# Performance work log

Hardware: AMD Instinct MI355X
Metric: run time of the kernel (lower is better)

## Reference

```python
import jax, jax.numpy as jnp
import numpy as np

D_MODEL = 2048
NUM_HEADS = 16
HEAD_DIM = D_MODEL // NUM_HEADS  # 128; scale uses head_dim even though attention is over full d_model
B, S = 2, 2048


def setup_inputs() -> dict:
    key = jax.random.key(0)
    ks = jax.random.split(key, 5)
    x = jax.random.normal(ks[0], (B, S, D_MODEL), dtype=jnp.float32)
    # causal additive mask, as typically passed to this module (2D, sliced mask[-s:, :kv])
    neg = jnp.float32(-1e9)
    mask = jnp.where(jnp.triu(jnp.ones((S, S), dtype=bool), k=1), neg, jnp.float32(0.0))
    std = 1.0 / np.sqrt(D_MODEL)
    Wq = jax.random.normal(ks[1], (D_MODEL, D_MODEL), dtype=jnp.float32) * std
    Wk = jax.random.normal(ks[2], (D_MODEL, D_MODEL), dtype=jnp.float32) * std
    Wv = jax.random.normal(ks[3], (D_MODEL, D_MODEL), dtype=jnp.float32) * std
    Wo = jax.random.normal(ks[4], (D_MODEL, D_MODEL), dtype=jnp.float32) * std
    return {"x": x, "mask": mask, "Wq": Wq, "Wk": Wk, "Wv": Wv, "Wo": Wo}


def reference(x, mask, Wq, Wk, Wv, Wo):
    # nn.Linear(bias=False): y = x @ W^T
    q = jnp.einsum('bsd,ed->bse', x, Wq)  # [B,S,D]
    k = jnp.einsum('bsd,ed->bse', x, Wk)
    v = jnp.einsum('bsd,ed->bse', x, Wv)
    scale = jnp.float32(HEAD_DIM ** -0.5)
    # NOTE: faithful to source — contraction over full d_model, no head split
    scores = jnp.einsum('bsd,btd->bst', q, k) * scale  # [B,S,S]
    scores = scores + mask  # mask[-s:, :kv] == mask here (s == kv)
    weights = jax.nn.softmax(scores, axis=-1)
    out = jnp.einsum('bst,btd->bsd', weights, v)
    return jnp.einsum('bsd,ed->bse', out, Wo)
```

## Files before the change

kernel.cpp:

```cpp
#include <hip/hip_runtime.h>

#define DM  2048
#define SQ  2048
#define NB  2
#define BSZ (NB * SQ)

typedef _Float16 f16x8 __attribute__((ext_vector_type(8)));
typedef __attribute__((ext_vector_type(4))) float f32x4;

#define ASG(p) (const __attribute__((address_space(1))) void*)(p)
#define ASL(p) (__attribute__((address_space(3))) void*)(p)

__device__ __forceinline__ unsigned short f2h(float f) {
  union { _Float16 h; unsigned short u; } x;
  x.h = (_Float16)f;
  return x.u;
}
__device__ __forceinline__ float h2f(unsigned short u) {
  union { unsigned short u; _Float16 h; } x;
  x.u = u;
  return (float)x.h;
}

__global__ __launch_bounds__(256) void cast_x_wo(const float4* __restrict__ x,
                                                 const float4* __restrict__ wo,
                                                 ushort4* __restrict__ outx,
                                                 ushort4* __restrict__ outwo,
                                                 int n4x, int n4w) {
  int i = blockIdx.x * 256 + threadIdx.x;
  float4 v;
  ushort4* dst;
  int j;
  if (i < n4x) { v = x[i]; dst = outx; j = i; }
  else { j = i - n4x; if (j >= n4w) return; v = wo[j]; dst = outwo; }
  ushort4 h;
  h.x = f2h(v.x); h.y = f2h(v.y); h.z = f2h(v.z); h.w = f2h(v.w);
  dst[j] = h;
}

__global__ __launch_bounds__(256) void cast_t(const float* __restrict__ wq,
                                              const float* __restrict__ wk,
                                              const float* __restrict__ wv,
                                              unsigned short* __restrict__ wqT,
                                              unsigned short* __restrict__ wkT,
                                              unsigned short* __restrict__ wvT) {
  __shared__ unsigned short tile[64][66];
  const float* in = (blockIdx.z == 0) ? wq : (blockIdx.z == 1) ? wk : wv;
  unsigned short* outT = (blockIdx.z == 0) ? wqT : (blockIdx.z == 1) ? wkT : wvT;
  const int tid = threadIdx.x;
  const int d0 = blockIdx.x * 64, e0 = blockIdx.y * 64;
  const int r = tid >> 4;
  const int c = (tid & 15) * 4;
#pragma unroll
  for (int p = 0; p < 4; p++) {
    const int dl = r + p * 16;
    float4 v = *(const float4*)&in[(long)(d0 + dl) * DM + e0 + c];
    tile[c + 0][dl] = f2h(v.x);
    tile[c + 1][dl] = f2h(v.y);
    tile[c + 2][dl] = f2h(v.z);
    tile[c + 3][dl] = f2h(v.w);
  }
  __syncthreads();
  const int r2 = tid >> 3;
  const int c2 = (tid & 7) * 8;
#pragma unroll
  for (int p = 0; p < 2; p++) {
    const int el = r2 + p * 32;
    union { uint4 u4; unsigned short us[8]; } o;
#pragma unroll
    for (int k = 0; k < 8; k++) o.us[k] = tile[el][c2 + k];
    *(uint4*)&outT[(long)(e0 + el) * DM + d0 + c2] = o.u4;
  }
}

#define SB() __builtin_amdgcn_sched_barrier(0)
#define BARX() do { SB(); __builtin_amdgcn_s_barrier(); SB(); } while (0)

#define STAGEK(BUFL, REG, U, T) do { \
    const unsigned short* G_ = (REG) ? Bb : Ab; \
    const int ldG_ = (REG) ? ldB : ldA; \
    const int r0_ = ((REG) ? bn0 : bm0) + (U) * 32; \
    const long k0_ = (long)((T) << 6); \
    char* db_ = ldsb + (BUFL) * 32768 + (REG) * 16384 + (U) * 4096 + tid * 16; \
    const unsigned short* s_ = G_ + (long)(r0_ + srow) * ldG_ + k0_ + scsw; \
    __builtin_amdgcn_global_load_lds(ASG(s_), ASL(db_), 16, 0, 0); \
  } while (0)

#define LDAK(BUFL, MH, Af) do { \
    const char* ba_ = ldsb + (BUFL) * 32768 + (wm * 64 + (MH) * 32) * 128 + arow; \
    _Pragma("unroll") for (int mm_ = 0; mm_ < 2; mm_++) { \
      Af[mm_][0] = *(const f16x8*)(ba_ + mm_ * 2048 + sl0); \
      Af[mm_][1] = *(const f16x8*)(ba_ + mm_ * 2048 + sl1); } \
  } while (0)

#define LDBK(BUFL, NH, Bf) do { \
    const char* bb_ = ldsb + (BUFL) * 32768 + 16384 + (wn * 64 + (NH) * 32) * 128 + arow; \
    _Pragma("unroll") for (int nn_ = 0; nn_ < 2; nn_++) { \
      Bf[nn_][0] = *(const f16x8*)(bb_ + nn_ * 2048 + sl0); \
      Bf[nn_][1] = *(const f16x8*)(bb_ + nn_ * 2048 + sl1); } \
  } while (0)

#define PHK(Af, Bf, MH, NH) do { \
    __builtin_amdgcn_s_setprio(1); \
    _Pragma("unroll") for (int mm_ = 0; mm_ < 2; mm_++) \
    _Pragma("unroll") for (int nn_ = 0; nn_ < 2; nn_++) \
    _Pragma("unroll") for (int ks_ = 0; ks_ < 2; ks_++) \
      acc[(MH) * 2 + mm_][(NH) * 2 + nn_] = __builtin_amdgcn_mfma_f32_16x16x32_f16( \
          Af[mm_][ks_], Bf[nn_][ks_], acc[(MH) * 2 + mm_][(NH) * 2 + nn_], 0, 0, 0); \
    __builtin_amdgcn_s_setprio(0); \
  } while (0)

#define GROUPK(BUFL, T) do { \
    LDAK(BUFL, 0, a0); LDBK(BUFL, 0, b0); \
    LDAK(BUFL, 1, a1); \
    if ((T) + 1 < NT) { STAGEK((BUFL) ^ 1, 1, 2, (T) + 1); STAGEK((BUFL) ^ 1, 1, 3, (T) + 1); } \
    PHK(a0, b0, 0, 0); \
    BARX(); \
    LDBK(BUFL, 1, b1); \
    PHK(a1, b0, 1, 0); \
    BARX(); \
    if ((T) + 2 < NT) { STAGEK(BUFL, 0, 0, (T) + 2); STAGEK(BUFL, 0, 1, (T) + 2); \
                        STAGEK(BUFL, 0, 2, (T) + 2); STAGEK(BUFL, 0, 3, (T) + 2); } \
    PHK(a1, b1, 1, 1); \
    BARX(); \
    if ((T) + 2 < NT) { STAGEK(BUFL, 1, 0, (T) + 2); STAGEK(BUFL, 1, 1, (T) + 2); } \
    PHK(a0, b1, 0, 1); \
    SB(); \
    if ((T) + 1 < NT) { \
      if ((T) + 1 == NT - 1) { asm volatile("s_waitcnt vmcnt(0)" ::: "memory"); } \
      else                   { asm volatile("s_waitcnt vmcnt(6)" ::: "memory"); } \
    } \
    __builtin_amdgcn_s_barrier(); \
    SB(); \
  } while (0)

template <int OM>
__device__ __forceinline__ void gemm128_body(
    char* ldsb, const unsigned short* __restrict__ Ab,
    const unsigned short* __restrict__ Bb,
    float* __restrict__ Cf, unsigned short* __restrict__ Ch, long cb,
    int NT, int ldA, int ldB, int ldC, int bm0, int bn0, float alpha) {
  const int tid = threadIdx.x, lane = tid & 63, wid = tid >> 6;
  const int wm = wid >> 1, wn = wid & 1;
  const int fr = lane & 15, fq = lane >> 4;

  const int sl0 = ((fq ^ (fr & 7)) << 4);
  const int sl1 = (((4 + fq) ^ (fr & 7)) << 4);
  const int arow = fr << 7;

  const int srow = tid >> 3;
  const int scsw = ((tid & 7) ^ (srow & 7)) << 3;

  f32x4 acc[4][4];
#pragma unroll
  for (int m = 0; m < 4; m++)
#pragma unroll
    for (int n = 0; n < 4; n++)
#pragma unroll
      for (int r = 0; r < 4; r++) acc[m][n][r] = 0.f;

  f16x8 a0[2][2], a1[2][2], b0[2][2], b1[2][2];

  STAGEK(0, 0, 0, 0); STAGEK(0, 0, 1, 0); STAGEK(0, 0, 2, 0); STAGEK(0, 0, 3, 0);
  STAGEK(0, 1, 0, 0); STAGEK(0, 1, 1, 0); STAGEK(0, 1, 2, 0); STAGEK(0, 1, 3, 0);
  STAGEK(1, 0, 0, 1); STAGEK(1, 0, 1, 1); STAGEK(1, 0, 2, 1); STAGEK(1, 0, 3, 1);
  STAGEK(1, 1, 0, 1); STAGEK(1, 1, 1, 1);
  asm volatile("s_waitcnt vmcnt(6)" ::: "memory");
  __builtin_amdgcn_s_barrier();
  SB();

  for (int t = 0; t < NT; t += 2) {
    GROUPK(0, t);
    GROUPK(1, t + 1);
  }

#pragma unroll
  for (int mh = 0; mh < 2; mh++)
#pragma unroll
    for (int mm = 0; mm < 2; mm++)
#pragma unroll
      for (int nh = 0; nh < 2; nh++)
#pragma unroll
        for (int nn = 0; nn < 2; nn++) {
          const int col = bn0 + wn * 64 + nh * 32 + nn * 16 + fr;
#pragma unroll
          for (int r = 0; r < 4; r++) {
            const long row = (long)bm0 + wm * 64 + mh * 32 + mm * 16 + fq * 4 + r;
            const long ci = cb + row * ldC + col;
            const float vv = acc[mh * 2 + mm][nh * 2 + nn][r] * alpha;
            if constexpr (OM == 0) Cf[ci] = vv;
            else                   Ch[ci] = f2h(vv);
          }
        }
}

template <int OM, int CAUSAL>
__global__ __launch_bounds__(256, 2) void gemm128(
    const unsigned short* __restrict__ A, const unsigned short* __restrict__ B,
    float* __restrict__ Cf, unsigned short* __restrict__ Ch,
    int K, long sAb, long sBb, long sCb,
    int ldA, int ldB, int ldC, float alpha) {
  __shared__ __align__(16) char ldsarr[65536];
  const int bm0 = blockIdx.x * 128;
  const int bn0 = blockIdx.y * 128;
  if (CAUSAL == 1 && bn0 > bm0) return;
  const int z = blockIdx.z;
  int NT = K >> 6;
  if (CAUSAL == 2) NT = (bm0 + 128) >> 6;
  gemm128_body<OM>(ldsarr, A + (long)z * sAb, B + (long)z * sBb,
                   Cf, Ch, (long)z * sCb, NT, ldA, ldB, ldC, bm0, bn0, alpha);
}

__global__ __launch_bounds__(256, 2) void k_mt_g(
    const unsigned short* __restrict__ wkT, const unsigned short* __restrict__ wqT,
    const unsigned short* __restrict__ wo16, const unsigned short* __restrict__ wvT,
    unsigned short* __restrict__ MT, unsigned short* __restrict__ G) {
  __shared__ __align__(16) char ldsarr[65536];
  const int bm0 = blockIdx.x * 128;
  const int bn0 = blockIdx.y * 128;
  if (blockIdx.z == 0)
    gemm128_body<1>(ldsarr, wkT, wqT, nullptr, MT, 0L, DM >> 6, DM, DM, DM, bm0, bn0, 1.0f);
  else
    gemm128_body<1>(ldsarr, wo16, wvT, nullptr, G, 0L, DM >> 6, DM, DM, DM, bm0, bn0, 1.0f);
}

__global__ __launch_bounds__(256, 2) void k_y_ut(
    const unsigned short* __restrict__ x16, const unsigned short* __restrict__ MT,
    const unsigned short* __restrict__ G,
    unsigned short* __restrict__ y, unsigned short* __restrict__ uT) {
  __shared__ __align__(16) char ldsarr[65536];
  if (blockIdx.z == 0) {
    const int bm0 = blockIdx.x * 128;
    const int bn0 = blockIdx.y * 128;
    gemm128_body<1>(ldsarr, x16, MT, nullptr, y, 0L, DM >> 6, DM, DM, DM, bm0, bn0, 1.0f);
  } else {
    const int bm0 = blockIdx.y * 128;
    const int bn0 = blockIdx.x * 128;
    gemm128_body<1>(ldsarr, G, x16, nullptr, uT, 0L, DM >> 6, DM, DM, BSZ, bm0, bn0, 1.0f);
  }
}

__global__ __launch_bounds__(256) void softmax_causal(const unsigned short* __restrict__ sc,
                                                      unsigned short* __restrict__ pr) {
  const int row = blockIdx.x;
  const int s = row & (SQ - 1);
  const long base = (long)row * SQ;
  const int n = s + 1;
  const int tid = threadIdx.x;
  const int lane = tid & 63;
  const int wv = tid >> 6;
  const int e0 = tid * 8;
  __shared__ float red[4];

  union { uint4 u4; unsigned short us[8]; } in, ou;
  in.u4 = *(const uint4*)&sc[base + e0];

  float v[8];
  float mx = -3.0e38f;
#pragma unroll
  for (int j = 0; j < 8; j++) {
    v[j] = (e0 + j < n) ? h2f(in.us[j]) : -3.0e38f;
    mx = fmaxf(mx, v[j]);
  }
#pragma unroll
  for (int o = 32; o >= 1; o >>= 1) mx = fmaxf(mx, __shfl_xor(mx, o));
  if (lane == 0) red[wv] = mx;
  __syncthreads();
  mx = fmaxf(fmaxf(red[0], red[1]), fmaxf(red[2], red[3]));
  __syncthreads();

  float sum = 0.f;
#pragma unroll
  for (int j = 0; j < 8; j++) {
    v[j] = (e0 + j < n) ? __expf(v[j] - mx) : 0.f;
    sum += v[j];
  }
#pragma unroll
  for (int o = 32; o >= 1; o >>= 1) sum += __shfl_xor(sum, o);
  if (lane == 0) red[wv] = sum;
  __syncthreads();
  const float inv = 1.f / (red[0] + red[1] + red[2] + red[3]);
#pragma unroll
  for (int j = 0; j < 8; j++) ou.us[j] = (e0 + j < n) ? f2h(v[j] * inv) : (unsigned short)0;
  *(uint4*)&pr[base + e0] = ou.u4;
}

extern "C" void kernel_launch(void* const* d_in, const int* in_sizes, int n_in,
                              void* d_out, int out_size, void* d_ws, size_t ws_size,
                              hipStream_t stream) {
  (void)in_sizes; (void)n_in; (void)out_size; (void)ws_size;
  const float* x  = (const float*)d_in[0];
  const float* Wq = (const float*)d_in[2];
  const float* Wk = (const float*)d_in[3];
  const float* Wv = (const float*)d_in[4];
  const float* Wo = (const float*)d_in[5];
  float* out = (float*)d_out;

  const long ELx = (long)BSZ * DM;
  const long ELw = (long)DM * DM;

  char* ws = (char*)d_ws;
  size_t off = 0;
  auto take = [&](size_t bytes) { void* p = ws + off; off += bytes; return p; };

  unsigned short* x16  = (unsigned short*)take(ELx * 2);
  unsigned short* wqT  = (unsigned short*)take(ELw * 2);
  unsigned short* wkT  = (unsigned short*)take(ELw * 2);
  unsigned short* wvT  = (unsigned short*)take(ELw * 2);
  unsigned short* wo16 = (unsigned short*)take(ELw * 2);
  unsigned short* MT   = (unsigned short*)take(ELw * 2);
  unsigned short* G    = (unsigned short*)take(ELw * 2);
  unsigned short* y    = (unsigned short*)take(ELx * 2);
  unsigned short* uT   = (unsigned short*)take(ELx * 2);
  unsigned short* probs = (unsigned short*)take((long)NB * SQ * SQ * 2);
  unsigned short* scores = wqT;

  const int n4x = (int)(ELx / 4), n4w = (int)(ELw / 4);
  cast_x_wo<<<dim3((n4x + n4w + 255) / 256), 256, 0, stream>>>(
      (const float4*)x, (const float4*)Wo, (ushort4*)x16, (ushort4*)wo16, n4x, n4w);
  cast_t<<<dim3(DM / 64, DM / 64, 3), 256, 0, stream>>>(
      Wq, Wk, Wv, wqT, wkT, wvT);

  const float scale = 0.08838834764831845f;

  k_mt_g<<<dim3(DM / 128, DM / 128, 2), 256, 0, stream>>>(
      wkT, wqT, wo16, wvT, MT, G);
  k_y_ut<<<dim3(BSZ / 128, DM / 128, 2), 256, 0, stream>>>(
      x16, MT, G, y, uT);
  gemm128<1, 1><<<dim3(SQ / 128, SQ / 128, NB), 256, 0, stream>>>(
      y, x16, nullptr, scores, DM, (long)SQ * DM, (long)SQ * DM,
      (long)SQ * SQ, DM, DM, SQ, scale);

  softmax_causal<<<dim3(NB * SQ), 256, 0, stream>>>(scores, probs);

  gemm128<0, 2><<<dim3(SQ / 128, DM / 128, NB), 256, 0, stream>>>(
      probs, uT, out, nullptr, SQ, (long)SQ * SQ, 2048L, (long)SQ * DM,
      SQ, BSZ, DM, 1.0f);
}
```

Before: 208.4 us.

## Split-K causal score GEMM over packed triangle tiles and pair PV row tiles

The causal score GEMM now launches only lower-triangle tiles, decoded from a linear block index with sqrt. Its K dimension is split in two halves written to separate fp16 buffers, and softmax sums the two halves on load. This removes the early-exit blocks and raises the block count to fill the GPU. The output GEMM pairs row tile xx with row tile 15-xx in one block so every block does equal causal work. The costs are an extra score buffer read in softmax, fp16 rounding applied to each partial sum, and a dependence on BARX and the reused wvT buffer being safe.

```diff
diff --git a/kernel.cpp b/kernel.cpp
--- a/kernel.cpp
+++ b/kernel.cpp
@@ -194,23 +194,6 @@
         }
 }
 
-template <int OM, int CAUSAL>
-__global__ __launch_bounds__(256, 2) void gemm128(
-    const unsigned short* __restrict__ A, const unsigned short* __restrict__ B,
-    float* __restrict__ Cf, unsigned short* __restrict__ Ch,
-    int K, long sAb, long sBb, long sCb,
-    int ldA, int ldB, int ldC, float alpha) {
-  __shared__ __align__(16) char ldsarr[65536];
-  const int bm0 = blockIdx.x * 128;
-  const int bn0 = blockIdx.y * 128;
-  if (CAUSAL == 1 && bn0 > bm0) return;
-  const int z = blockIdx.z;
-  int NT = K >> 6;
-  if (CAUSAL == 2) NT = (bm0 + 128) >> 6;
-  gemm128_body<OM>(ldsarr, A + (long)z * sAb, B + (long)z * sBb,
-                   Cf, Ch, (long)z * sCb, NT, ldA, ldB, ldC, bm0, bn0, alpha);
-}
-
 __global__ __launch_bounds__(256, 2) void k_mt_g(
     const unsigned short* __restrict__ wkT, const unsigned short* __restrict__ wqT,
     const unsigned short* __restrict__ wo16, const unsigned short* __restrict__ wvT,
@@ -240,7 +223,42 @@
   }
 }
 
-__global__ __launch_bounds__(256) void softmax_causal(const unsigned short* __restrict__ sc,
+__global__ __launch_bounds__(256, 2) void k_scores2(
+    const unsigned short* __restrict__ y, const unsigned short* __restrict__ x16,
+    unsigned short* __restrict__ slo, unsigned short* __restrict__ shi,
+    float scale) {
+  __shared__ __align__(16) char ldsarr[65536];
+  const int b = blockIdx.x;
+  const int u = b % 136;
+  const int zh = b / 136;
+  const long z = zh & 1;
+  const int h = zh >> 1;
+  const int r = (int)((sqrtf(8.f * (float)u + 1.f) - 1.f) * 0.5f);
+  const int c = u - ((r * (r + 1)) >> 1);
+  const unsigned short* Ab = y   + z * (long)SQ * DM + h * 1024;
+  const unsigned short* Bb = x16 + z * (long)SQ * DM + h * 1024;
+  gemm128_body<1>(ldsarr, Ab, Bb, nullptr, h ? shi : slo,
+                  z * (long)SQ * SQ, 16, DM, DM, SQ, r * 128, c * 128, scale);
+}
+
+__global__ __launch_bounds__(256, 2) void k_out(
+    const unsigned short* __restrict__ probs, const unsigned short* __restrict__ uT,
+    float* __restrict__ out) {
+  __shared__ __align__(16) char ldsarr[65536];
+  const int xx = blockIdx.x;
+  const int bn0 = blockIdx.y * 128;
+  const long z = blockIdx.z;
+  const unsigned short* Ab = probs + z * (long)SQ * SQ;
+  const unsigned short* Bb = uT + z * 2048;
+  gemm128_body<0>(ldsarr, Ab, Bb, out, nullptr, z * (long)SQ * DM,
+                  2 * (xx + 1), SQ, BSZ, DM, 128 * xx, bn0, 1.0f);
+  BARX();
+  gemm128_body<0>(ldsarr, Ab, Bb, out, nullptr, z * (long)SQ * DM,
+                  2 * (16 - xx), SQ, BSZ, DM, 128 * (15 - xx), bn0, 1.0f);
+}
+
+__global__ __launch_bounds__(256) void softmax_causal(const unsigned short* __restrict__ lo,
+                                                      const unsigned short* __restrict__ hi,
                                                       unsigned short* __restrict__ pr) {
   const int row = blockIdx.x;
   const int s = row & (SQ - 1);
@@ -252,14 +270,15 @@
   const int e0 = tid * 8;
   __shared__ float red[4];
 
-  union { uint4 u4; unsigned short us[8]; } in, ou;
-  in.u4 = *(const uint4*)&sc[base + e0];
+  union { uint4 u4; unsigned short us[8]; } i1, i2, ou;
+  i1.u4 = *(const uint4*)&lo[base + e0];
+  i2.u4 = *(const uint4*)&hi[base + e0];
 
   float v[8];
   float mx = -3.0e38f;
 #pragma unroll
   for (int j = 0; j < 8; j++) {
-    v[j] = (e0 + j < n) ? h2f(in.us[j]) : -3.0e38f;
+    v[j] = (e0 + j < n) ? (h2f(i1.us[j]) + h2f(i2.us[j])) : -3.0e38f;
     mx = fmaxf(mx, v[j]);
   }
 #pragma unroll
@@ -313,7 +332,8 @@
   unsigned short* y    = (unsigned short*)take(ELx * 2);
   unsigned short* uT   = (unsigned short*)take(ELx * 2);
   unsigned short* probs = (unsigned short*)take((long)NB * SQ * SQ * 2);
-  unsigned short* scores = wqT;
+  unsigned short* slo = wqT;
+  unsigned short* shi = wvT;
 
   const int n4x = (int)(ELx / 4), n4w = (int)(ELw / 4);
   cast_x_wo<<<dim3((n4x + n4w + 255) / 256), 256, 0, stream>>>(
@@ -327,13 +347,9 @@
       wkT, wqT, wo16, wvT, MT, G);
   k_y_ut<<<dim3(BSZ / 128, DM / 128, 2), 256, 0, stream>>>(
       x16, MT, G, y, uT);
-  gemm128<1, 1><<<dim3(SQ / 128, SQ / 128, NB), 256, 0, stream>>>(
-      y, x16, nullptr, scores, DM, (long)SQ * DM, (long)SQ * DM,
-      (long)SQ * SQ, DM, DM, SQ, scale);
-
-  softmax_causal<<<dim3(NB * SQ), 256, 0, stream>>>(scores, probs);
-
-  gemm128<0, 2><<<dim3(SQ / 128, DM / 128, NB), 256, 0, stream>>>(
-      probs, uT, out, nullptr, SQ, (long)SQ * SQ, 2048L, (long)SQ * DM,
-      SQ, BSZ, DM, 1.0f);
-}
+  k_scores2<<<dim3(544, 1, 1), 256, 0, stream>>>(y, x16, slo, shi, scale);
+
+  softmax_causal<<<dim3(NB * SQ), 256, 0, stream>>>(slo, shi, probs);
+
+  k_out<<<dim3(8, DM / 128, NB), 256, 0, stream>>>(probs, uT, out);
+}
```

New measurement: 214.9 us. 1.03x slower.
